# Kernel optimization log

Hardware: AMD Instinct MI355X
Metric: run time of the kernel (lower is better)

Reference implementation:

```python
import jax, jax.numpy as jnp
import numpy as np

# NOTE: the original torch code writes `torch.tensor(10 ^ -18)` which is Python
# bitwise XOR, i.e. the constant -28 (NOT 1e-18). We replicate that exact math.
RULE_OFFSET = -28.0


def setup_inputs() -> dict:
    key = jax.random.key(0)
    k0, k1, k2, k3 = jax.random.split(key, 4)
    batch, n_rules, n_fea = 8192, 256, 128
    data = jax.random.normal(k0, (batch, n_fea), dtype=jnp.float32)
    para_mu = jax.random.uniform(k1, (n_rules, n_fea), dtype=jnp.float32)
    para_sigma = jax.random.uniform(k2, (n_rules, n_fea), dtype=jnp.float32)
    para_w3 = jax.random.uniform(k3, (n_rules, n_fea + 1), dtype=jnp.float32)
    return {"data": data, "para_mu": para_mu, "para_sigma": para_sigma, "para_w3": para_w3}


def reference(data, para_mu, para_sigma, para_w3):
    # Gaussian fuzzification exponents: (batch, n_rules, n_fea)
    diff = data[:, None, :] - para_mu[None, :, :]
    exponent = -(diff ** 2) / (2.0 * para_sigma ** 2)
    # prod over features of exp(.) == exp(sum over features) -- same math, fused.
    layer_rule = jnp.exp(jnp.sum(exponent, axis=2))  # (batch, n_rules)
    layer_rule = layer_rule + RULE_OFFSET
    inv_frn = 1.0 / jnp.sum(layer_rule, axis=1, keepdims=True)  # (batch, 1)
    layer_normalize = layer_rule * inv_frn  # (batch, n_rules)
    # TSK consequent: w3[:,0] + sum_f w3[:,1:] * x
    layer_conq = para_w3[:, 0][None, :] + jnp.einsum('bf,rf->br', data, para_w3[:, 1:])
    layer_out_tsk = jnp.sum(layer_normalize * layer_conq, axis=1)  # (batch,)
    return jax.nn.sigmoid(layer_out_tsk)
```

## Files before the change

### kernel.cpp

```cpp
#include <hip/hip_runtime.h>
#include <math.h>

#define NR 256
#define NF 128
#define BCOLS 32

typedef short  s16x8  __attribute__((ext_vector_type(8)));
typedef __bf16 bf16x8 __attribute__((ext_vector_type(8)));
typedef float  f32x16 __attribute__((ext_vector_type(16)));

__device__ __forceinline__ unsigned short f2bf(float x) {
    unsigned int u = __float_as_uint(x);
    unsigned int r = (u + 0x7FFFu + ((u >> 16) & 1u)) >> 16;
    return (unsigned short)r;
}
__device__ __forceinline__ float bf2f(unsigned short b) {
    return __uint_as_float(((unsigned int)b) << 16);
}
__device__ __forceinline__ bf16x8 as_bf(s16x8 v) {
    return __builtin_bit_cast(bf16x8, v);
}
__device__ __forceinline__ f32x16 mfma_bf16(s16x8 a, s16x8 b, f32x16 acc) {
    return __builtin_amdgcn_mfma_f32_32x32x16_bf16(as_bf(a), as_bf(b), acc, 0, 0, 0);
}

__global__ __launch_bounds__(256) void prep2_kernel(
    const float* __restrict__ mu, const float* __restrict__ sigma,
    const float* __restrict__ w3,
    unsigned short* __restrict__ PH, unsigned short* __restrict__ PL,
    unsigned short* __restrict__ WC,
    float* __restrict__ Cr, float* __restrict__ W0)
{
    const int blk = blockIdx.x;
    if (blk < 32) {
        const int t    = blk * 256 + threadIdx.x;
        const int e    = t >> 6;
        const int lane = t & 63;
        const int rt   = e >> 4;
        const int ks2  = e & 15;
        const bool second = (ks2 >= 8);
        const int fb   = (ks2 & 7) * 16 + (lane >> 5) * 8;
        const int rule = rt * 32 + (lane & 31);

        const float* mrow = mu    + (size_t)rule * NF + fb;
        const float* srow = sigma + (size_t)rule * NF + fb;
        const float* wrow = w3    + (size_t)rule * (NF + 1) + 1 + fb;

        s16x8 vh, vl, vw;
        #pragma unroll
        for (int j = 0; j < 8; ++j) {
            const float s  = srow[j];
            const float m  = mrow[j];
            const float w  = wrow[j];
            const float u2 = -0.5f / fmaxf(s * s, 1e-30f);
            const float val = second ? (-2.0f * u2 * m) : u2;
            const unsigned short hh = f2bf(val);
            vh[j] = (short)hh;
            vl[j] = (short)f2bf(val - bf2f(hh));
            const unsigned short wh = f2bf(w);
            vw[j] = (short)(second ? f2bf(w - bf2f(wh)) : wh);
        }
        ((s16x8*)PH)[t] = vh;
        ((s16x8*)PL)[t] = vl;
        ((s16x8*)WC)[t] = vw;
    } else {
        const int rg   = blk - 32;
        const int rl   = threadIdx.x >> 3;
        const int jj   = threadIdx.x & 7;
        const int rule = rg * 32 + rl;
        const float* mrow = mu    + (size_t)rule * NF + jj * 16;
        const float* srow = sigma + (size_t)rule * NF + jj * 16;
        float cc = 0.f;
        #pragma unroll
        for (int q = 0; q < 16; q += 4) {
            const float4 s4 = *(const float4*)(srow + q);
            const float4 m4 = *(const float4*)(mrow + q);
            cc += (-0.5f / fmaxf(s4.x * s4.x, 1e-30f)) * m4.x * m4.x;
            cc += (-0.5f / fmaxf(s4.y * s4.y, 1e-30f)) * m4.y * m4.y;
            cc += (-0.5f / fmaxf(s4.z * s4.z, 1e-30f)) * m4.z * m4.z;
            cc += (-0.5f / fmaxf(s4.w * s4.w, 1e-30f)) * m4.w * m4.w;
        }
        cc += __shfl_down(cc, 4);
        cc += __shfl_down(cc, 2);
        cc += __shfl_down(cc, 1);
        if (jj == 0) {
            Cr[rule] = cc;
            W0[rule] = w3[(size_t)rule * (NF + 1)];
        }
    }
}

__global__ __launch_bounds__(512) void fnn_mfma(
    const float* __restrict__ data,
    const unsigned short* __restrict__ PH, const unsigned short* __restrict__ PL,
    const unsigned short* __restrict__ WC,
    const float* __restrict__ Cr, const float* __restrict__ W0,
    float* __restrict__ out)
{
    __shared__ s16x8 sBH[16][64], sBL[16][64];
    __shared__ float sCr[NR], sW0[NR];
    __shared__ float redD[8][BCOLS], redN[8][BCOLS];

    const int tid = threadIdx.x;
    if (tid < NR) sCr[tid] = Cr[tid];
    else          sW0[tid - NR] = W0[tid - NR];

    const int b0 = blockIdx.x * BCOLS;

    {
        const int bks = tid >> 6;
        const int bln = tid & 63;
        const float* p = data + (size_t)(b0 + (bln & 31)) * NF
                              + bks * 16 + (bln >> 5) * 8;
        const float4 v0 = *(const float4*)(p);
        const float4 v1 = *(const float4*)(p + 4);
        const float dv[8] = {v0.x, v0.y, v0.z, v0.w, v1.x, v1.y, v1.z, v1.w};
        s16x8 e_d, e_dl, e_d2, e_d2l;
        #pragma unroll
        for (int j = 0; j < 8; ++j) {
            const float d  = dv[j];
            const float d2 = d * d;
            const unsigned short dh  = f2bf(d);
            const unsigned short d2h = f2bf(d2);
            e_d  [j] = (short)dh;
            e_dl [j] = (short)f2bf(d  - bf2f(dh));
            e_d2 [j] = (short)d2h;
            e_d2l[j] = (short)f2bf(d2 - bf2f(d2h));
        }
        sBH[bks    ][bln] = e_d2;
        sBL[bks    ][bln] = e_d2l;
        sBH[bks + 8][bln] = e_d;
        sBL[bks + 8][bln] = e_dl;
    }
    __syncthreads();

    const int wv   = tid >> 6;
    const int lane = tid & 63;
    const int col  = lane & 31;
    const int half = lane >> 5;

    const s16x8* PHp = (const s16x8*)PH + (size_t)wv * 16 * 64 + lane;
    const s16x8* PLp = (const s16x8*)PL + (size_t)wv * 16 * 64 + lane;
    const s16x8* WCp = (const s16x8*)WC + (size_t)wv * 16 * 64 + lane;

    f32x16 accS0, accS1, accQ;
    #pragma unroll
    for (int e = 0; e < 16; ++e) { accS0[e] = 0.f; accS1[e] = 0.f; accQ[e] = 0.f; }

    s16x8 a0 = PHp[0], a1 = PLp[0], a2 = WCp[0];
    #pragma unroll 1
    for (int ks = 0; ks < 16; ++ks) {
        const int nofs = ((ks < 15) ? (ks + 1) : ks) * 64;
        const s16x8 n0 = PHp[nofs];
        const s16x8 n1 = PLp[nofs];
        const s16x8 n2 = WCp[nofs];

        const s16x8 bh = sBH[ks][lane];
        const s16x8 bl = sBL[ks][lane];
        accS0 = mfma_bf16(a0, bh, accS0);
        accS1 = mfma_bf16(a1, bh, accS1);
        accS1 = mfma_bf16(a0, bl, accS1);
        if (ks < 8) {
            accQ = mfma_bf16(a2, sBH[ks + 8][lane], accQ);
            accQ = mfma_bf16(a2, sBL[ks + 8][lane], accQ);
        } else {
            accQ = mfma_bf16(a2, bh, accQ);
        }
        a0 = n0; a1 = n1; a2 = n2;
    }

    float den_p = 0.f, num_p = 0.f;
    #pragma unroll
    for (int reg = 0; reg < 16; ++reg) {
        const int rloc = (reg & 3) + 8 * (reg >> 2) + 4 * half;
        const int rule = wv * 32 + rloc;
        const float S  = accS0[reg] + accS1[reg] + sCr[rule];
        const float rv = __expf(fminf(S, 0.f)) - 28.0f;
        const float cq = accQ[reg] + sW0[rule];
        den_p += rv;
        num_p += rv * cq;
    }
    den_p += __shfl_xor(den_p, 32);
    num_p += __shfl_xor(num_p, 32);
    if (half == 0) { redD[wv][col] = den_p; redN[wv][col] = num_p; }
    __syncthreads();

    if (tid < BCOLS) {
        float den = 0.f, num = 0.f;
        #pragma unroll
        for (int w = 0; w < 8; ++w) { den += redD[w][tid]; num += redN[w][tid]; }
        out[b0 + tid] = 1.0f / (1.0f + __expf(-(num / den)));
    }
}

#define TBF 8
__global__ __launch_bounds__(256) void fnn_fused(
    const float* __restrict__ data,
    const float* __restrict__ mu, const float* __restrict__ sigma,
    const float* __restrict__ w3,
    float* __restrict__ out)
{
    __shared__ float d_tile[TBF][NF];
    __shared__ float red[TBF][2][4];

    const int tid = threadIdx.x;
    const int b0  = blockIdx.x * TBF;
    {
        const float4* src = (const float4*)(data + (size_t)b0 * NF);
        ((float4*)(&d_tile[0][0]))[tid] = src[tid];
    }
    __syncthreads();

    const float* mu_r = mu    + (size_t)tid * NF;
    const float* sg_r = sigma + (size_t)tid * NF;
    const float* w_r  = w3    + (size_t)tid * (NF + 1);

    float S[TBF], Q[TBF];
    #pragma unroll
    for (int b = 0; b < TBF; ++b) { S[b] = 0.f; Q[b] = 0.f; }

    #pragma unroll 2
    for (int f = 0; f < NF; f += 4) {
        const float4 m4 = *(const float4*)(mu_r + f);
        const float4 s4 = *(const float4*)(sg_r + f);
        const float w0 = w_r[1 + f + 0], w1 = w_r[1 + f + 1];
        const float w2 = w_r[1 + f + 2], w3v = w_r[1 + f + 3];
        float4 c4;
        c4.x = -0.5f / fmaxf(s4.x * s4.x, 1e-30f);
        c4.y = -0.5f / fmaxf(s4.y * s4.y, 1e-30f);
        c4.z = -0.5f / fmaxf(s4.z * s4.z, 1e-30f);
        c4.w = -0.5f / fmaxf(s4.w * s4.w, 1e-30f);
        #pragma unroll
        for (int b = 0; b < TBF; ++b) {
            const float4 d4 = *(const float4*)(&d_tile[b][f]);
            float t;
            t = d4.x - m4.x; S[b] = fmaf(t * t, c4.x, S[b]); Q[b] = fmaf(d4.x, w0,  Q[b]);
            t = d4.y - m4.y; S[b] = fmaf(t * t, c4.y, S[b]); Q[b] = fmaf(d4.y, w1,  Q[b]);
            t = d4.z - m4.z; S[b] = fmaf(t * t, c4.z, S[b]); Q[b] = fmaf(d4.z, w2,  Q[b]);
            t = d4.w - m4.w; S[b] = fmaf(t * t, c4.w, S[b]); Q[b] = fmaf(d4.w, w3v, Q[b]);
        }
    }

    const float bias = w_r[0];
    #pragma unroll
    for (int b = 0; b < TBF; ++b) {
        float rule = __expf(S[b]) - 28.0f;
        float rc   = rule * (bias + Q[b]);
        #pragma unroll
        for (int off = 32; off > 0; off >>= 1) {
            rule += __shfl_down(rule, off);
            rc   += __shfl_down(rc,   off);
        }
        if ((tid & 63) == 0) {
            red[b][0][tid >> 6] = rule;
            red[b][1][tid >> 6] = rc;
        }
    }
    __syncthreads();
    if (tid < TBF) {
        const float den = red[tid][0][0] + red[tid][0][1] + red[tid][0][2] + red[tid][0][3];
        const float num = red[tid][1][0] + red[tid][1][1] + red[tid][1][2] + red[tid][1][3];
        out[b0 + tid] = 1.0f / (1.0f + __expf(-(num / den)));
    }
}

extern "C" void kernel_launch(void* const* d_in, const int* in_sizes, int n_in,
                              void* d_out, int out_size, void* d_ws, size_t ws_size,
                              hipStream_t stream) {
    const float* data  = (const float*)d_in[0];
    const float* mu    = (const float*)d_in[1];
    const float* sigma = (const float*)d_in[2];
    const float* w3    = (const float*)d_in[3];
    float* out = (float*)d_out;

    const int batch = in_sizes[0] / NF;
    const size_t need = 3u * 65536u * sizeof(unsigned short) + 2u * NR * sizeof(float);

    if (ws_size >= need && (batch % BCOLS) == 0) {
        unsigned short* PH = (unsigned short*)d_ws;
        unsigned short* PL = PH + 65536;
        unsigned short* WC = PL + 65536;
        float* Cr = (float*)(WC + 65536);
        float* W0 = Cr + NR;
        prep2_kernel<<<40, 256, 0, stream>>>(mu, sigma, w3, PH, PL, WC, Cr, W0);
        fnn_mfma<<<batch / BCOLS, 512, 0, stream>>>(data, PH, PL, WC, Cr, W0, out);
    } else {
        fnn_fused<<<batch / TBF, 256, 0, stream>>>(data, mu, sigma, w3, out);
    }
}
```

Baseline: 18.26 us.

## Fully unroll MFMA k-loop with double-buffered 4-step global prefetch groups

Replaces the unroll-1 k-loop, which prefetched one step ahead, with a fully unrolled sequence. The A operands (PH, PL, WC) are loaded in groups of four k-steps into two alternating register sets, and sched_barrier keeps the compiler from reordering loads across groups. The aim is more global loads in flight and less latency exposed between MFMAs, plus no loop overhead or branch on ks. The cost is higher VGPR use (24 s16x8 registers), which could lower occupancy.

```diff
diff --git a/kernel.cpp b/kernel.cpp
--- a/kernel.cpp
+++ b/kernel.cpp
@@ -147,27 +147,70 @@
     #pragma unroll
     for (int e = 0; e < 16; ++e) { accS0[e] = 0.f; accS1[e] = 0.f; accQ[e] = 0.f; }
 
-    s16x8 a0 = PHp[0], a1 = PLp[0], a2 = WCp[0];
-    #pragma unroll 1
-    for (int ks = 0; ks < 16; ++ks) {
-        const int nofs = ((ks < 15) ? (ks + 1) : ks) * 64;
-        const s16x8 n0 = PHp[nofs];
-        const s16x8 n1 = PLp[nofs];
-        const s16x8 n2 = WCp[nofs];
-
-        const s16x8 bh = sBH[ks][lane];
-        const s16x8 bl = sBL[ks][lane];
-        accS0 = mfma_bf16(a0, bh, accS0);
-        accS1 = mfma_bf16(a1, bh, accS1);
-        accS1 = mfma_bf16(a0, bl, accS1);
-        if (ks < 8) {
-            accQ = mfma_bf16(a2, sBH[ks + 8][lane], accQ);
-            accQ = mfma_bf16(a2, sBL[ks + 8][lane], accQ);
-        } else {
-            accQ = mfma_bf16(a2, bh, accQ);
-        }
-        a0 = n0; a1 = n1; a2 = n2;
-    }
+    s16x8 X0h, X0l, X0w, X1h, X1l, X1w, X2h, X2l, X2w, X3h, X3l, X3w;
+    s16x8 Y0h, Y0l, Y0w, Y1h, Y1l, Y1w, Y2h, Y2l, Y2w, Y3h, Y3l, Y3w;
+
+#define LOADX(G) \
+    X0h = PHp[((G)*4+0)*64]; X0l = PLp[((G)*4+0)*64]; X0w = WCp[((G)*4+0)*64]; \
+    X1h = PHp[((G)*4+1)*64]; X1l = PLp[((G)*4+1)*64]; X1w = WCp[((G)*4+1)*64]; \
+    X2h = PHp[((G)*4+2)*64]; X2l = PLp[((G)*4+2)*64]; X2w = WCp[((G)*4+2)*64]; \
+    X3h = PHp[((G)*4+3)*64]; X3l = PLp[((G)*4+3)*64]; X3w = WCp[((G)*4+3)*64];
+#define LOADY(G) \
+    Y0h = PHp[((G)*4+0)*64]; Y0l = PLp[((G)*4+0)*64]; Y0w = WCp[((G)*4+0)*64]; \
+    Y1h = PHp[((G)*4+1)*64]; Y1l = PLp[((G)*4+1)*64]; Y1w = WCp[((G)*4+1)*64]; \
+    Y2h = PHp[((G)*4+2)*64]; Y2l = PLp[((G)*4+2)*64]; Y2w = WCp[((G)*4+2)*64]; \
+    Y3h = PHp[((G)*4+3)*64]; Y3l = PLp[((G)*4+3)*64]; Y3w = WCp[((G)*4+3)*64];
+
+#define KS_LO(AH, AL, AW, KS)                        \
+    {                                                 \
+        const s16x8 bh = sBH[KS][lane];               \
+        const s16x8 bl = sBL[KS][lane];               \
+        const s16x8 qh = sBH[(KS) + 8][lane];         \
+        const s16x8 ql = sBL[(KS) + 8][lane];         \
+        accS0 = mfma_bf16(AH, bh, accS0);             \
+        accS1 = mfma_bf16(AL, bh, accS1);             \
+        accS1 = mfma_bf16(AH, bl, accS1);             \
+        accQ  = mfma_bf16(AW, qh, accQ);              \
+        accQ  = mfma_bf16(AW, ql, accQ);              \
+    }
+#define KS_HI(AH, AL, AW, KS)                        \
+    {                                                 \
+        const s16x8 bh = sBH[KS][lane];               \
+        const s16x8 bl = sBL[KS][lane];               \
+        accS0 = mfma_bf16(AH, bh, accS0);             \
+        accS1 = mfma_bf16(AL, bh, accS1);             \
+        accS1 = mfma_bf16(AH, bl, accS1);             \
+        accQ  = mfma_bf16(AW, bh, accQ);              \
+    }
+
+    LOADX(0)
+    LOADY(1)
+    KS_LO(X0h, X0l, X0w, 0)
+    KS_LO(X1h, X1l, X1w, 1)
+    KS_LO(X2h, X2l, X2w, 2)
+    KS_LO(X3h, X3l, X3w, 3)
+    __builtin_amdgcn_sched_barrier(0);
+    LOADX(2)
+    KS_LO(Y0h, Y0l, Y0w, 4)
+    KS_LO(Y1h, Y1l, Y1w, 5)
+    KS_LO(Y2h, Y2l, Y2w, 6)
+    KS_LO(Y3h, Y3l, Y3w, 7)
+    __builtin_amdgcn_sched_barrier(0);
+    LOADY(3)
+    KS_HI(X0h, X0l, X0w, 8)
+    KS_HI(X1h, X1l, X1w, 9)
+    KS_HI(X2h, X2l, X2w, 10)
+    KS_HI(X3h, X3l, X3w, 11)
+    __builtin_amdgcn_sched_barrier(0);
+    KS_HI(Y0h, Y0l, Y0w, 12)
+    KS_HI(Y1h, Y1l, Y1w, 13)
+    KS_HI(Y2h, Y2l, Y2w, 14)
+    KS_HI(Y3h, Y3l, Y3w, 15)
+
+#undef LOADX
+#undef LOADY
+#undef KS_LO
+#undef KS_HI
 
     float den_p = 0.f, num_p = 0.f;
     #pragma unroll
```

After: 17.43 us. -4.6%, faster.

## Process two 32-column batch tiles per block to reuse rule-parameter fragments

Applied to the files above, without the earlier changes.

Each block now handles 64 batch rows instead of 32, loading each A fragment (PH, PL, WC) from global once and applying it to two B tiles held in shared memory. This halves the global parameter traffic per batch row and doubles the MFMA work per load, which improves the ratio of compute to memory. In exchange it doubles the accumulator registers and shared-memory footprint, and halves the grid to 128 blocks, which may leave some of the many CUs idle.

```diff
diff --git a/kernel.cpp b/kernel.cpp
--- a/kernel.cpp
+++ b/kernel.cpp
@@ -3,7 +3,7 @@
 
 #define NR 256
 #define NF 128
-#define BCOLS 32
+#define BCOLS 64
 
 typedef short  s16x8  __attribute__((ext_vector_type(8)));
 typedef __bf16 bf16x8 __attribute__((ext_vector_type(8)));
@@ -97,7 +97,7 @@
     const float* __restrict__ Cr, const float* __restrict__ W0,
     float* __restrict__ out)
 {
-    __shared__ s16x8 sBH[16][64], sBL[16][64];
+    __shared__ s16x8 sBH[16][128], sBL[16][128];
     __shared__ float sCr[NR], sW0[NR];
     __shared__ float redD[8][BCOLS], redN[8][BCOLS];
 
@@ -110,27 +110,31 @@
     {
         const int bks = tid >> 6;
         const int bln = tid & 63;
-        const float* p = data + (size_t)(b0 + (bln & 31)) * NF
-                              + bks * 16 + (bln >> 5) * 8;
-        const float4 v0 = *(const float4*)(p);
-        const float4 v1 = *(const float4*)(p + 4);
-        const float dv[8] = {v0.x, v0.y, v0.z, v0.w, v1.x, v1.y, v1.z, v1.w};
-        s16x8 e_d, e_dl, e_d2, e_d2l;
-        #pragma unroll
-        for (int j = 0; j < 8; ++j) {
-            const float d  = dv[j];
-            const float d2 = d * d;
-            const unsigned short dh  = f2bf(d);
-            const unsigned short d2h = f2bf(d2);
-            e_d  [j] = (short)dh;
-            e_dl [j] = (short)f2bf(d  - bf2f(dh));
-            e_d2 [j] = (short)d2h;
-            e_d2l[j] = (short)f2bf(d2 - bf2f(d2h));
-        }
-        sBH[bks    ][bln] = e_d2;
-        sBL[bks    ][bln] = e_d2l;
-        sBH[bks + 8][bln] = e_d;
-        sBL[bks + 8][bln] = e_dl;
+        #pragma unroll
+        for (int tile = 0; tile < 2; ++tile) {
+            const float* p = data + (size_t)(b0 + tile * 32 + (bln & 31)) * NF
+                                  + bks * 16 + (bln >> 5) * 8;
+            const float4 v0 = *(const float4*)(p);
+            const float4 v1 = *(const float4*)(p + 4);
+            const float dv[8] = {v0.x, v0.y, v0.z, v0.w, v1.x, v1.y, v1.z, v1.w};
+            s16x8 e_d, e_dl, e_d2, e_d2l;
+            #pragma unroll
+            for (int j = 0; j < 8; ++j) {
+                const float d  = dv[j];
+                const float d2 = d * d;
+                const unsigned short dh  = f2bf(d);
+                const unsigned short d2h = f2bf(d2);
+                e_d  [j] = (short)dh;
+                e_dl [j] = (short)f2bf(d  - bf2f(dh));
+                e_d2 [j] = (short)d2h;
+                e_d2l[j] = (short)f2bf(d2 - bf2f(d2h));
+            }
+            const int o = tile * 64 + bln;
+            sBH[bks    ][o] = e_d2;
+            sBL[bks    ][o] = e_d2l;
+            sBH[bks + 8][o] = e_d;
+            sBL[bks + 8][o] = e_dl;
+        }
     }
     __syncthreads();
 
@@ -143,9 +147,12 @@
     const s16x8* PLp = (const s16x8*)PL + (size_t)wv * 16 * 64 + lane;
     const s16x8* WCp = (const s16x8*)WC + (size_t)wv * 16 * 64 + lane;
 
-    f32x16 accS0, accS1, accQ;
+    f32x16 accS0a, accS1a, accQa, accS0b, accS1b, accQb;
     #pragma unroll
-    for (int e = 0; e < 16; ++e) { accS0[e] = 0.f; accS1[e] = 0.f; accQ[e] = 0.f; }
+    for (int e = 0; e < 16; ++e) {
+        accS0a[e] = 0.f; accS1a[e] = 0.f; accQa[e] = 0.f;
+        accS0b[e] = 0.f; accS1b[e] = 0.f; accQb[e] = 0.f;
+    }
 
     s16x8 a0 = PHp[0], a1 = PLp[0], a2 = WCp[0];
     #pragma unroll 1
@@ -155,34 +162,52 @@
         const s16x8 n1 = PLp[nofs];
         const s16x8 n2 = WCp[nofs];
 
-        const s16x8 bh = sBH[ks][lane];
-        const s16x8 bl = sBL[ks][lane];
-        accS0 = mfma_bf16(a0, bh, accS0);
-        accS1 = mfma_bf16(a1, bh, accS1);
-        accS1 = mfma_bf16(a0, bl, accS1);
+        const s16x8 bh0 = sBH[ks][lane];
+        const s16x8 bl0 = sBL[ks][lane];
+        const s16x8 bh1 = sBH[ks][64 + lane];
+        const s16x8 bl1 = sBL[ks][64 + lane];
+        accS0a = mfma_bf16(a0, bh0, accS0a);
+        accS1a = mfma_bf16(a1, bh0, accS1a);
+        accS1a = mfma_bf16(a0, bl0, accS1a);
+        accS0b = mfma_bf16(a0, bh1, accS0b);
+        accS1b = mfma_bf16(a1, bh1, accS1b);
+        accS1b = mfma_bf16(a0, bl1, accS1b);
         if (ks < 8) {
-            accQ = mfma_bf16(a2, sBH[ks + 8][lane], accQ);
-            accQ = mfma_bf16(a2, sBL[ks + 8][lane], accQ);
+            accQa = mfma_bf16(a2, sBH[ks + 8][lane], accQa);
+            accQa = mfma_bf16(a2, sBL[ks + 8][lane], accQa);
+            accQb = mfma_bf16(a2, sBH[ks + 8][64 + lane], accQb);
+            accQb = mfma_bf16(a2, sBL[ks + 8][64 + lane], accQb);
         } else {
-            accQ = mfma_bf16(a2, bh, accQ);
+            accQa = mfma_bf16(a2, bh0, accQa);
+            accQb = mfma_bf16(a2, bh1, accQb);
         }
         a0 = n0; a1 = n1; a2 = n2;
     }
 
-    float den_p = 0.f, num_p = 0.f;
+    float denA = 0.f, numA = 0.f, denB = 0.f, numB = 0.f;
     #pragma unroll
     for (int reg = 0; reg < 16; ++reg) {
         const int rloc = (reg & 3) + 8 * (reg >> 2) + 4 * half;
         const int rule = wv * 32 + rloc;
-        const float S  = accS0[reg] + accS1[reg] + sCr[rule];
-        const float rv = __expf(fminf(S, 0.f)) - 28.0f;
-        const float cq = accQ[reg] + sW0[rule];
-        den_p += rv;
-        num_p += rv * cq;
-    }
-    den_p += __shfl_xor(den_p, 32);
-    num_p += __shfl_xor(num_p, 32);
-    if (half == 0) { redD[wv][col] = den_p; redN[wv][col] = num_p; }
+        const float cr = sCr[rule];
+        const float w0 = sW0[rule];
+        const float Sa  = accS0a[reg] + accS1a[reg] + cr;
+        const float rva = __expf(fminf(Sa, 0.f)) - 28.0f;
+        denA += rva;
+        numA += rva * (accQa[reg] + w0);
+        const float Sb  = accS0b[reg] + accS1b[reg] + cr;
+        const float rvb = __expf(fminf(Sb, 0.f)) - 28.0f;
+        denB += rvb;
+        numB += rvb * (accQb[reg] + w0);
+    }
+    denA += __shfl_xor(denA, 32);
+    numA += __shfl_xor(numA, 32);
+    denB += __shfl_xor(denB, 32);
+    numB += __shfl_xor(numB, 32);
+    if (half == 0) {
+        redD[wv][col]      = denA;  redN[wv][col]      = numA;
+        redD[wv][32 + col] = denB;  redN[wv][32 + col] = numB;
+    }
     __syncthreads();
 
     if (tid < BCOLS) {
```

Measured after the change: 20.56 us. 1.13x slower.

## Split rule dimension across grid blocks with partial sums and a finish kernel

Applied to the files above, without the earlier changes.

Adds a split kernel where each block covers 128 batch columns and 64 rules, so each wave reuses its rule-tile A fragments across 64 batch columns and the rule parameters are loaded fewer times per batch element. Partial denominators and numerators go to workspace and a separate finish kernel combines them and applies the sigmoid. This trades reloading the parameter tiles for one extra kernel launch and a global round trip for the partial sums. The original path stays as a fallback when the workspace is too small.

```diff
diff --git a/kernel.cpp b/kernel.cpp
--- a/kernel.cpp
+++ b/kernel.cpp
@@ -3,7 +3,6 @@
 
 #define NR 256
 #define NF 128
-#define BCOLS 32
 
 typedef short  s16x8  __attribute__((ext_vector_type(8)));
 typedef __bf16 bf16x8 __attribute__((ext_vector_type(8)));
@@ -90,6 +89,138 @@
     }
 }
 
+__global__ __launch_bounds__(512) void fnn_mfma_split(
+    const float* __restrict__ data,
+    const unsigned short* __restrict__ PH, const unsigned short* __restrict__ PL,
+    const unsigned short* __restrict__ WC,
+    const float* __restrict__ Cr, const float* __restrict__ W0,
+    float* __restrict__ pden, float* __restrict__ pnum, int batch)
+{
+    __shared__ s16x8 sBH[16][256], sBL[16][256];
+    __shared__ float sCr[64], sW0[64];
+    __shared__ float redD[8][32], redN[8][32];
+
+    const int tid = threadIdx.x;
+    const int bt128 = blockIdx.x;
+    const int rg    = blockIdx.y;
+    const int b0    = bt128 * 128;
+    const int rbase = rg * 64;
+
+    if (tid < 64)        sCr[tid]      = Cr[rbase + tid];
+    else if (tid < 128)  sW0[tid - 64] = W0[rbase + tid - 64];
+
+    {
+        const int bks = tid >> 6;
+        const int bln = tid & 63;
+        #pragma unroll
+        for (int t4 = 0; t4 < 4; ++t4) {
+            const float* p = data + (size_t)(b0 + t4 * 32 + (bln & 31)) * NF
+                                  + bks * 16 + (bln >> 5) * 8;
+            const float4 v0 = *(const float4*)(p);
+            const float4 v1 = *(const float4*)(p + 4);
+            const float dv[8] = {v0.x, v0.y, v0.z, v0.w, v1.x, v1.y, v1.z, v1.w};
+            s16x8 e_d, e_dl, e_d2, e_d2l;
+            #pragma unroll
+            for (int j = 0; j < 8; ++j) {
+                const float d  = dv[j];
+                const float d2 = d * d;
+                const unsigned short dh  = f2bf(d);
+                const unsigned short d2h = f2bf(d2);
+                e_d  [j] = (short)dh;
+                e_dl [j] = (short)f2bf(d  - bf2f(dh));
+                e_d2 [j] = (short)d2h;
+                e_d2l[j] = (short)f2bf(d2 - bf2f(d2h));
+            }
+            const int o = t4 * 64 + bln;
+            sBH[bks    ][o] = e_d2;
+            sBL[bks    ][o] = e_d2l;
+            sBH[bks + 8][o] = e_d;
+            sBL[bks + 8][o] = e_dl;
+        }
+    }
+    __syncthreads();
+
+    const int wv   = tid >> 6;
+    const int lane = tid & 63;
+    const int col  = lane & 31;
+    const int half = lane >> 5;
+    const int rt_l = wv & 1;
+    const int bt   = wv >> 1;
+    const int rtile = rg * 2 + rt_l;
+    const int bo   = bt * 64;
+
+    const s16x8* PHp = (const s16x8*)PH + (size_t)rtile * 1024 + lane;
+    const s16x8* PLp = (const s16x8*)PL + (size_t)rtile * 1024 + lane;
+    const s16x8* WCp = (const s16x8*)WC + (size_t)rtile * 1024 + lane;
+
+    f32x16 accS0, accS1, accQ;
+    #pragma unroll
+    for (int e = 0; e < 16; ++e) { accS0[e] = 0.f; accS1[e] = 0.f; accQ[e] = 0.f; }
+
+    s16x8 a0 = PHp[0], a1 = PLp[0], a2 = WCp[0];
+    #pragma unroll 1
+    for (int ks = 0; ks < 16; ++ks) {
+        const int nofs = ((ks < 15) ? (ks + 1) : ks) * 64;
+        const s16x8 n0 = PHp[nofs];
+        const s16x8 n1 = PLp[nofs];
+        const s16x8 n2 = WCp[nofs];
+
+        const s16x8 bh = sBH[ks][bo + lane];
+        const s16x8 bl = sBL[ks][bo + lane];
+        accS0 = mfma_bf16(a0, bh, accS0);
+        accS1 = mfma_bf16(a1, bh, accS1);
+        accS1 = mfma_bf16(a0, bl, accS1);
+        if (ks < 8) {
+            accQ = mfma_bf16(a2, sBH[ks + 8][bo + lane], accQ);
+            accQ = mfma_bf16(a2, sBL[ks + 8][bo + lane], accQ);
+        } else {
+            accQ = mfma_bf16(a2, bh, accQ);
+        }
+        a0 = n0; a1 = n1; a2 = n2;
+    }
+
+    float den_p = 0.f, num_p = 0.f;
+    #pragma unroll
+    for (int reg = 0; reg < 16; ++reg) {
+        const int rloc = (reg & 3) + 8 * (reg >> 2) + 4 * half;
+        const int rl64 = rt_l * 32 + rloc;
+        const float S  = accS0[reg] + accS1[reg] + sCr[rl64];
+        const float rv = __expf(fminf(S, 0.f)) - 28.0f;
+        const float cq = accQ[reg] + sW0[rl64];
+        den_p += rv;
+        num_p += rv * cq;
+    }
+    den_p += __shfl_xor(den_p, 32);
+    num_p += __shfl_xor(num_p, 32);
+    if (half == 0) { redD[wv][col] = den_p; redN[wv][col] = num_p; }
+    __syncthreads();
+
+    if (tid < 128) {
+        const int c  = tid;
+        const int sb = c >> 5, cl = c & 31;
+        const float den = redD[2 * sb][cl] + redD[2 * sb + 1][cl];
+        const float num = redN[2 * sb][cl] + redN[2 * sb + 1][cl];
+        pden[(size_t)rg * batch + b0 + c] = den;
+        pnum[(size_t)rg * batch + b0 + c] = num;
+    }
+}
+
+__global__ __launch_bounds__(256) void fnn_finish(
+    const float* __restrict__ pden, const float* __restrict__ pnum,
+    float* __restrict__ out, int batch)
+{
+    const int b = blockIdx.x * 256 + threadIdx.x;
+    if (b < batch) {
+        float den = 0.f, num = 0.f;
+        #pragma unroll
+        for (int g = 0; g < 4; ++g) {
+            den += pden[(size_t)g * batch + b];
+            num += pnum[(size_t)g * batch + b];
+        }
+        out[b] = 1.0f / (1.0f + __expf(-(num / den)));
+    }
+}
+
 __global__ __launch_bounds__(512) void fnn_mfma(
     const float* __restrict__ data,
     const unsigned short* __restrict__ PH, const unsigned short* __restrict__ PL,
@@ -99,13 +230,13 @@
 {
     __shared__ s16x8 sBH[16][64], sBL[16][64];
     __shared__ float sCr[NR], sW0[NR];
-    __shared__ float redD[8][BCOLS], redN[8][BCOLS];
+    __shared__ float redD[8][32], redN[8][32];
 
     const int tid = threadIdx.x;
     if (tid < NR) sCr[tid] = Cr[tid];
     else          sW0[tid - NR] = W0[tid - NR];
 
-    const int b0 = blockIdx.x * BCOLS;
+    const int b0 = blockIdx.x * 32;
 
     {
         const int bks = tid >> 6;
@@ -139,9 +270,9 @@
     const int col  = lane & 31;
     const int half = lane >> 5;
 
-    const s16x8* PHp = (const s16x8*)PH + (size_t)wv * 16 * 64 + lane;
-    const s16x8* PLp = (const s16x8*)PL + (size_t)wv * 16 * 64 + lane;
-    const s16x8* WCp = (const s16x8*)WC + (size_t)wv * 16 * 64 + lane;
+    const s16x8* PHp = (const s16x8*)PH + (size_t)wv * 1024 + lane;
+    const s16x8* PLp = (const s16x8*)PL + (size_t)wv * 1024 + lane;
+    const s16x8* WCp = (const s16x8*)WC + (size_t)wv * 1024 + lane;
 
     f32x16 accS0, accS1, accQ;
     #pragma unroll
@@ -185,7 +316,7 @@
     if (half == 0) { redD[wv][col] = den_p; redN[wv][col] = num_p; }
     __syncthreads();
 
-    if (tid < BCOLS) {
+    if (tid < 32) {
         float den = 0.f, num = 0.f;
         #pragma unroll
         for (int w = 0; w < 8; ++w) { den += redD[w][tid]; num += redN[w][tid]; }
@@ -274,16 +405,27 @@
     float* out = (float*)d_out;
 
     const int batch = in_sizes[0] / NF;
-    const size_t need = 3u * 65536u * sizeof(unsigned short) + 2u * NR * sizeof(float);
-
-    if (ws_size >= need && (batch % BCOLS) == 0) {
-        unsigned short* PH = (unsigned short*)d_ws;
-        unsigned short* PL = PH + 65536;
-        unsigned short* WC = PL + 65536;
-        float* Cr = (float*)(WC + 65536);
-        float* W0 = Cr + NR;
+    const size_t need_base  = 3u * 65536u * sizeof(unsigned short)
+                            + 2u * NR * sizeof(float);
+    const size_t need_split = need_base + (size_t)8 * batch * sizeof(float);
+
+    unsigned short* PH = (unsigned short*)d_ws;
+    unsigned short* PL = PH + 65536;
+    unsigned short* WC = PL + 65536;
+    float* Cr = (float*)(WC + 65536);
+    float* W0 = Cr + NR;
+    float* pden = W0 + NR;
+    float* pnum = pden + (size_t)4 * batch;
+
+    if (ws_size >= need_split && (batch % 128) == 0 && (batch % 256) == 0) {
         prep2_kernel<<<40, 256, 0, stream>>>(mu, sigma, w3, PH, PL, WC, Cr, W0);
-        fnn_mfma<<<batch / BCOLS, 512, 0, stream>>>(data, PH, PL, WC, Cr, W0, out);
+        dim3 grid(batch / 128, 4);
+        fnn_mfma_split<<<grid, 512, 0, stream>>>(data, PH, PL, WC, Cr, W0,
+                                                 pden, pnum, batch);
+        fnn_finish<<<batch / 256, 256, 0, stream>>>(pden, pnum, out, batch);
+    } else if (ws_size >= need_base && (batch % 32) == 0) {
+        prep2_kernel<<<40, 256, 0, stream>>>(mu, sigma, w3, PH, PL, WC, Cr, W0);
+        fnn_mfma<<<batch / 32, 512, 0, stream>>>(data, PH, PL, WC, Cr, W0, out);
     } else {
         fnn_fused<<<batch / TBF, 256, 0, stream>>>(data, mu, sigma, w3, out);
     }
```

Result: slower. 21.23 us (+16.3%).
